# Kernel tuning notes

Measured on AMD Instinct MI355X. Metric: run time of the kernel, lower is better.

Reference implementation:

```python
import jax, jax.numpy as jnp
import numpy as np

EPS = 1e-5  # torch LayerNorm default

def _layernorm(x, g, b):
    mu = jnp.mean(x, axis=-1, keepdims=True)
    var = jnp.var(x, axis=-1, keepdims=True)
    return (x - mu) * jax.lax.rsqrt(var + EPS) * g + b

def _mlp(x, g, b, W1, b1, W2, b2):
    # pre-norm LayerNorm -> Linear -> SiLU -> Linear
    h = _layernorm(x, g, b)
    h = jax.nn.silu(h @ W1 + b1)
    return h @ W2 + b2

N, B, F, H = 500_000, 25_000, 128, 64

def setup_inputs() -> dict:
    key = jax.random.key(0)
    ks = jax.random.split(key, 16)
    s = 0.05
    return {
        "pos": jax.random.normal(ks[0], (N, 3), jnp.float32),
        "mass_center": jax.random.normal(ks[1], (B, 3), jnp.float32),
        "scaler": jax.random.normal(ks[2], (N, F), jnp.float32),
        "vector": jax.random.normal(ks[3], (N, 3, F), jnp.float32),
        "batch_index": jnp.sort(jax.random.randint(ks[4], (N,), 0, B)),
        # decoder_alpha params (pre-norm MLP F->H->1)
        "ln_a_g": jnp.ones((F,), jnp.float32),
        "ln_a_b": jnp.zeros((F,), jnp.float32),
        "Wa1": jax.random.normal(ks[5], (F, H), jnp.float32) * s,
        "ba1": jnp.zeros((H,), jnp.float32),
        "Wa2": jax.random.normal(ks[6], (H, 1), jnp.float32) * s,
        "ba2": jnp.zeros((1,), jnp.float32),
        # decoder_nu: gate MLP (pre-norm, F->H->1) + bias-free Linear(F,1)
        "ln_n_g": jnp.ones((F,), jnp.float32),
        "ln_n_b": jnp.zeros((F,), jnp.float32),
        "Wn1": jax.random.normal(ks[7], (F, H), jnp.float32) * s,
        "bn1": jnp.zeros((H,), jnp.float32),
        "Wn2": jax.random.normal(ks[8], (H, 1), jnp.float32) * s,
        "bn2": jnp.zeros((1,), jnp.float32),
        "Wnu": jax.random.normal(ks[9], (F, 1), jnp.float32) * s,
    }

def reference(pos, mass_center, scaler, vector, batch_index,
              ln_a_g, ln_a_b, Wa1, ba1, Wa2, ba2,
              ln_n_g, ln_n_b, Wn1, bn1, Wn2, bn2, Wnu):
    # gather per-node mass center and center positions: [N,3]
    mcv = pos - mass_center[batch_index]
    # Gate: mlp(scaler) [N,1] broadcast-multiplied with vector @ Wnu [N,3,1]
    s_gate = _mlp(scaler, ln_n_g, ln_n_b, Wn1, bn1, Wn2, bn2)       # [N,1]
    v_proj = jnp.einsum('ndf,fo->ndo', vector, Wnu)                  # [N,3,1]
    nu = (s_gate[:, None, :] * v_proj)[..., 0]                       # [N,3]
    # symmetric outer products: [N,3,3]
    outer = nu[:, :, None] * mcv[:, None, :] + mcv[:, :, None] * nu[:, None, :]
    alpha_s = _mlp(scaler, ln_a_g, ln_a_b, Wa1, ba1, Wa2, ba2)       # [N,1]
    alpha = alpha_s[:, :, None] * jnp.eye(3, dtype=alpha_s.dtype) + outer  # [N,3,3]
    # scatter-sum to molecule level, then trace/3
    mol = jax.ops.segment_sum(alpha, batch_index, num_segments=B)    # [B,3,3]
    out = jnp.einsum('bii->b', mol) / 3.0
    return out[:, None]                                              # [B,1]
```

## Files before the change

### kernel.cpp

```cpp
#include <hip/hip_runtime.h>

#define FD 128
#define HD 64
#define NC 128
#define RPB 64

typedef __attribute__((ext_vector_type(8))) short bf16x8;
typedef __attribute__((ext_vector_type(4))) float f32x4;

__device__ __forceinline__ unsigned bfr(float x) {
    unsigned u = __float_as_uint(x);
    return (u + 0x7fffu + ((u >> 16) & 1u)) >> 16;
}

__global__ void prep_kernel(
    const float* __restrict__ lnag, const float* __restrict__ lnab,
    const float* __restrict__ Wa1, const float* __restrict__ ba1, const float* __restrict__ Wa2,
    const float* __restrict__ lnng, const float* __restrict__ lnnb,
    const float* __restrict__ Wn1, const float* __restrict__ bn1, const float* __restrict__ Wn2,
    unsigned short* __restrict__ wq, float* __restrict__ c, float* __restrict__ w2)
{
    int n = threadIdx.x;
    const float* W  = (n < HD) ? Wa1 : Wn1;
    const float* g  = (n < HD) ? lnag : lnng;
    const float* bb = (n < HD) ? lnab : lnnb;
    const float* b1 = (n < HD) ? ba1 : bn1;
    const float* W2 = (n < HD) ? Wa2 : Wn2;
    int h = n & (HD - 1);
    float accb = b1[h];
    for (int f = 0; f < FD; ++f) {
        float w = W[f * HD + h];
        wq[n * FD + f] = (unsigned short)bfr(g[f] * w);
        accb += bb[f] * w;
    }
    c[n] = accb;
    w2[n] = W2[h];
}

__global__ __launch_bounds__(256) void fused_kernel(
    const float* __restrict__ scaler, const float* __restrict__ vec,
    const float* __restrict__ wnu, const float* __restrict__ pos,
    const float* __restrict__ mc, const int* __restrict__ bidx,
    const unsigned short* __restrict__ wq, const float* __restrict__ c,
    const float* __restrict__ w2, const float* __restrict__ ba2,
    const float* __restrict__ bn2, float* __restrict__ out, int n_nodes)
{
    __shared__ uint4 xs[RPB * 16];
    __shared__ float tl[RPB];

    int tid = threadIdx.x;
    int rowbase = blockIdx.x * RPB;
    int lane = tid & 63, w = tid >> 6;

    {
        int h = lane >> 5, j = lane & 31;
        float4 wn = reinterpret_cast<const float4*>(wnu)[j];
#pragma unroll
        for (int it = 0; it < 8; ++it) {
            int nl = w * 16 + it * 2 + h;
            int node = rowbase + nl;
            bool valid = node < n_nodes;
            int n = valid ? node : (n_nodes - 1);
            int b = bidx[n];
            float m0 = pos[n * 3 + 0] - mc[b * 3 + 0];
            float m1 = pos[n * 3 + 1] - mc[b * 3 + 1];
            float m2 = pos[n * 3 + 2] - mc[b * 3 + 2];
            const float4* vr = reinterpret_cast<const float4*>(vec + (size_t)n * 3 * FD);
            float4 v0 = vr[j], v1 = vr[32 + j], v2 = vr[64 + j];
            float acc = (v0.x * wn.x + v0.y * wn.y + v0.z * wn.z + v0.w * wn.w) * m0
                      + (v1.x * wn.x + v1.y * wn.y + v1.z * wn.z + v1.w * wn.w) * m1
                      + (v2.x * wn.x + v2.y * wn.y + v2.z * wn.z + v2.w * wn.w) * m2;
#pragma unroll
            for (int off = 16; off; off >>= 1) acc += __shfl_xor(acc, off);
            if (j == 0 && valid) tl[nl] = acc;
        }
    }

    {
        int r = tid >> 2, qd = tid & 3;
        int node = rowbase + r;
        int gn = node < n_nodes ? node : (n_nodes - 1);
        const float4* rp = reinterpret_cast<const float4*>(scaler + (size_t)gn * FD) + qd * 8;
        float4 v[8];
        float s = 0.f, s2 = 0.f;
#pragma unroll
        for (int i = 0; i < 8; ++i) {
            v[i] = rp[i];
            s  += v[i].x + v[i].y + v[i].z + v[i].w;
            s2 += v[i].x * v[i].x + v[i].y * v[i].y + v[i].z * v[i].z + v[i].w * v[i].w;
        }
        s  += __shfl_xor(s, 1);  s  += __shfl_xor(s, 2);
        s2 += __shfl_xor(s2, 1); s2 += __shfl_xor(s2, 2);
        float mu = s * (1.f / FD);
        float var = s2 * (1.f / FD) - mu * mu;
        float rstd = rsqrtf(var + 1e-5f);
#pragma unroll
        for (int jj = 0; jj < 4; ++jj) {
            float4 a = v[2 * jj], b = v[2 * jj + 1];
            uint4 pk;
            pk.x = bfr((a.x - mu) * rstd) | (bfr((a.y - mu) * rstd) << 16);
            pk.y = bfr((a.z - mu) * rstd) | (bfr((a.w - mu) * rstd) << 16);
            pk.z = bfr((b.x - mu) * rstd) | (bfr((b.y - mu) * rstd) << 16);
            pk.w = bfr((b.z - mu) * rstd) | (bfr((b.w - mu) * rstd) << 16);
            int slot = qd * 4 + jj;
            xs[r * 16 + (slot ^ (r & 15))] = pk;
        }
    }
    __syncthreads();

    int lrow = lane & 15, lgrp = lane >> 4;
    bf16x8 af[4];
#pragma unroll
    for (int ks = 0; ks < 4; ++ks) {
        int r = w * 16 + lrow;
        af[ks] = *reinterpret_cast<const bf16x8*>(&xs[r * 16 + ((ks * 4 + lgrp) ^ (r & 15))]);
    }
    float pa[4] = {0.f, 0.f, 0.f, 0.f}, pn[4] = {0.f, 0.f, 0.f, 0.f};
#pragma unroll
    for (int tile = 0; tile < 8; ++tile) {
        f32x4 acc = {0.f, 0.f, 0.f, 0.f};
        int n = tile * 16 + lrow;
        const bf16x8* brow = reinterpret_cast<const bf16x8*>(wq + n * FD);
#pragma unroll
        for (int ks = 0; ks < 4; ++ks) {
            bf16x8 bf = brow[ks * 4 + lgrp];
            acc = __builtin_amdgcn_mfma_f32_16x16x32_bf16(af[ks], bf, acc, 0, 0, 0);
        }
        int col = tile * 16 + lrow;
        float bias = c[col], w2v = w2[col];
#pragma unroll
        for (int r = 0; r < 4; ++r) {
            float h1 = acc[r] + bias;
            float y = h1 / (1.f + __expf(-h1));
            float cb = y * w2v;
            if (tile < 4) pa[r] += cb; else pn[r] += cb;
        }
    }
#pragma unroll
    for (int off = 1; off < 16; off <<= 1) {
#pragma unroll
        for (int r = 0; r < 4; ++r) {
            pa[r] += __shfl_xor(pa[r], off);
            pn[r] += __shfl_xor(pn[r], off);
        }
    }
    if (lrow == 0) {
        float b2a = ba2[0], b2n = bn2[0];
#pragma unroll
        for (int r = 0; r < 4; ++r) {
            int nl = w * 16 + lgrp * 4 + r;
            int node = rowbase + nl;
            if (node < n_nodes) {
                float val = (pa[r] + b2a) + (2.f / 3.f) * (pn[r] + b2n) * tl[nl];
                atomicAdd(out + bidx[node], val);
            }
        }
    }
}

extern "C" void kernel_launch(void* const* d_in, const int* in_sizes, int n_in,
                              void* d_out, int out_size, void* d_ws, size_t ws_size,
                              hipStream_t stream) {
    const float* pos    = (const float*)d_in[0];
    const float* mc     = (const float*)d_in[1];
    const float* scaler = (const float*)d_in[2];
    const float* vec    = (const float*)d_in[3];
    const int*   bidx   = (const int*)d_in[4];
    const float* lnag   = (const float*)d_in[5];
    const float* lnab   = (const float*)d_in[6];
    const float* Wa1    = (const float*)d_in[7];
    const float* ba1    = (const float*)d_in[8];
    const float* Wa2    = (const float*)d_in[9];
    const float* ba2    = (const float*)d_in[10];
    const float* lnng   = (const float*)d_in[11];
    const float* lnnb   = (const float*)d_in[12];
    const float* Wn1    = (const float*)d_in[13];
    const float* bn1    = (const float*)d_in[14];
    const float* Wn2    = (const float*)d_in[15];
    const float* bn2    = (const float*)d_in[16];
    const float* Wnu    = (const float*)d_in[17];

    int N = in_sizes[0] / 3;
    int B = in_sizes[1] / 3;

    unsigned short* wq = (unsigned short*)d_ws;
    float* c  = (float*)((char*)d_ws + NC * FD * 2);
    float* w2 = c + NC;

    hipMemsetAsync(d_out, 0, (size_t)B * sizeof(float), stream);

    hipLaunchKernelGGL(prep_kernel, dim3(1), dim3(NC), 0, stream,
                       lnag, lnab, Wa1, ba1, Wa2, lnng, lnnb, Wn1, bn1, Wn2, wq, c, w2);

    int blocks = (N + RPB - 1) / RPB;
    hipLaunchKernelGGL(fused_kernel, dim3(blocks), dim3(256), 0, stream,
                       scaler, vec, Wnu, pos, mc, bidx, wq, c, w2, ba2, bn2,
                       (float*)d_out, N);
}
```

Before: 277.6 us.

## Warp-specialize fused kernel into producer/consumer waves over persistent blocks

Turns the fused kernel into a persistent grid of 512 blocks with 512 threads each. Six producer waves stream the vector tensor and compute the per-node vector projection into a double-buffered shared slot. Two consumer waves do the LayerNorm, the MFMA MLP and the atomics, each handling 32 rows. The aim is to overlap the bandwidth-heavy vector reads with the scaler and MLP work and to cut per-block launch overhead. In exchange, only two waves now do all the scaler loads and MFMA work, occupancy drops to one block per CU, and every tile adds a block-wide barrier.

```diff
diff --git a/kernel.cpp b/kernel.cpp
--- a/kernel.cpp
+++ b/kernel.cpp
@@ -4,6 +4,8 @@
 #define HD 64
 #define NC 128
 #define RPB 64
+#define NPROD 6
+#define NBLK 512
 
 typedef __attribute__((ext_vector_type(8))) short bf16x8;
 typedef __attribute__((ext_vector_type(4))) float f32x4;
@@ -37,48 +39,43 @@
     w2[n] = W2[h];
 }
 
-__global__ __launch_bounds__(256) void fused_kernel(
-    const float* __restrict__ scaler, const float* __restrict__ vec,
-    const float* __restrict__ wnu, const float* __restrict__ pos,
-    const float* __restrict__ mc, const int* __restrict__ bidx,
-    const unsigned short* __restrict__ wq, const float* __restrict__ c,
-    const float* __restrict__ w2, const float* __restrict__ ba2,
-    const float* __restrict__ bn2, float* __restrict__ out, int n_nodes)
-{
-    __shared__ uint4 xs[RPB * 16];
-    __shared__ float tl[RPB];
-
-    int tid = threadIdx.x;
-    int rowbase = blockIdx.x * RPB;
-    int lane = tid & 63, w = tid >> 6;
-
-    {
-        int h = lane >> 5, j = lane & 31;
-        float4 wn = reinterpret_cast<const float4*>(wnu)[j];
-#pragma unroll
-        for (int it = 0; it < 8; ++it) {
-            int nl = w * 16 + it * 2 + h;
-            int node = rowbase + nl;
-            bool valid = node < n_nodes;
-            int n = valid ? node : (n_nodes - 1);
-            int b = bidx[n];
-            float m0 = pos[n * 3 + 0] - mc[b * 3 + 0];
-            float m1 = pos[n * 3 + 1] - mc[b * 3 + 1];
-            float m2 = pos[n * 3 + 2] - mc[b * 3 + 2];
-            const float4* vr = reinterpret_cast<const float4*>(vec + (size_t)n * 3 * FD);
-            float4 v0 = vr[j], v1 = vr[32 + j], v2 = vr[64 + j];
-            float acc = (v0.x * wn.x + v0.y * wn.y + v0.z * wn.z + v0.w * wn.w) * m0
-                      + (v1.x * wn.x + v1.y * wn.y + v1.z * wn.z + v1.w * wn.w) * m1
-                      + (v2.x * wn.x + v2.y * wn.y + v2.z * wn.z + v2.w * wn.w) * m2;
-#pragma unroll
-            for (int off = 16; off; off >>= 1) acc += __shfl_xor(acc, off);
-            if (j == 0 && valid) tl[nl] = acc;
-        }
-    }
-
-    {
-        int r = tid >> 2, qd = tid & 3;
-        int node = rowbase + r;
+__device__ __forceinline__ void produce_tile(
+    int tilebase, float* __restrict__ tslot,
+    const float* __restrict__ vec, const float4 wn,
+    const float* __restrict__ pos, const float* __restrict__ mc,
+    const int* __restrict__ bidx, int n_nodes, int hw, int j)
+{
+    for (int slot = hw; slot < RPB; slot += 2 * NPROD) {
+        int node = tilebase + slot;
+        bool valid = node < n_nodes;
+        int n = valid ? node : (n_nodes - 1);
+        const float4* vr = reinterpret_cast<const float4*>(vec + (size_t)n * 3 * FD);
+        float4 v0 = vr[j], v1 = vr[32 + j], v2 = vr[64 + j];
+        int b = bidx[n];
+        float m0 = pos[n * 3 + 0] - mc[b * 3 + 0];
+        float m1 = pos[n * 3 + 1] - mc[b * 3 + 1];
+        float m2 = pos[n * 3 + 2] - mc[b * 3 + 2];
+        float acc = (v0.x * wn.x + v0.y * wn.y + v0.z * wn.z + v0.w * wn.w) * m0
+                  + (v1.x * wn.x + v1.y * wn.y + v1.z * wn.z + v1.w * wn.w) * m1
+                  + (v2.x * wn.x + v2.y * wn.y + v2.z * wn.z + v2.w * wn.w) * m2;
+#pragma unroll
+        for (int off = 16; off; off >>= 1) acc += __shfl_xor(acc, off);
+        if (j == 0 && valid) tslot[slot] = acc;
+    }
+}
+
+__device__ __forceinline__ void consume_tile(
+    int tilebase, const float* __restrict__ tslot, uint4* __restrict__ xs,
+    const float* __restrict__ scaler, const unsigned short* __restrict__ wq,
+    const float* __restrict__ c, const float* __restrict__ w2,
+    float b2a, float b2n, const int* __restrict__ bidx,
+    float* __restrict__ out, int n_nodes, int cw, int lane)
+{
+    int r16 = lane >> 2, qd = lane & 3;
+#pragma unroll
+    for (int g = 0; g < 2; ++g) {
+        int row = cw * 32 + g * 16 + r16;
+        int node = tilebase + row;
         int gn = node < n_nodes ? node : (n_nodes - 1);
         const float4* rp = reinterpret_cast<const float4*>(scaler + (size_t)gn * FD) + qd * 8;
         float4 v[8];
@@ -103,57 +100,109 @@
             pk.z = bfr((b.x - mu) * rstd) | (bfr((b.y - mu) * rstd) << 16);
             pk.w = bfr((b.z - mu) * rstd) | (bfr((b.w - mu) * rstd) << 16);
             int slot = qd * 4 + jj;
-            xs[r * 16 + (slot ^ (r & 15))] = pk;
-        }
-    }
-    __syncthreads();
-
+            xs[row * 16 + (slot ^ (row & 15))] = pk;
+        }
+    }
     int lrow = lane & 15, lgrp = lane >> 4;
-    bf16x8 af[4];
+    bf16x8 af0[4], af1[4];
+    int r0 = cw * 32 + lrow, r1 = r0 + 16;
 #pragma unroll
     for (int ks = 0; ks < 4; ++ks) {
-        int r = w * 16 + lrow;
-        af[ks] = *reinterpret_cast<const bf16x8*>(&xs[r * 16 + ((ks * 4 + lgrp) ^ (r & 15))]);
-    }
-    float pa[4] = {0.f, 0.f, 0.f, 0.f}, pn[4] = {0.f, 0.f, 0.f, 0.f};
-#pragma unroll
-    for (int tile = 0; tile < 8; ++tile) {
-        f32x4 acc = {0.f, 0.f, 0.f, 0.f};
-        int n = tile * 16 + lrow;
+        af0[ks] = *reinterpret_cast<const bf16x8*>(&xs[r0 * 16 + ((ks * 4 + lgrp) ^ (r0 & 15))]);
+        af1[ks] = *reinterpret_cast<const bf16x8*>(&xs[r1 * 16 + ((ks * 4 + lgrp) ^ (r1 & 15))]);
+    }
+    float pa0[4] = {0,0,0,0}, pn0[4] = {0,0,0,0}, pa1[4] = {0,0,0,0}, pn1[4] = {0,0,0,0};
+#pragma unroll
+    for (int tc = 0; tc < 8; ++tc) {
+        f32x4 a0 = {0.f,0.f,0.f,0.f}, a1 = {0.f,0.f,0.f,0.f};
+        int n = tc * 16 + lrow;
         const bf16x8* brow = reinterpret_cast<const bf16x8*>(wq + n * FD);
 #pragma unroll
         for (int ks = 0; ks < 4; ++ks) {
             bf16x8 bf = brow[ks * 4 + lgrp];
-            acc = __builtin_amdgcn_mfma_f32_16x16x32_bf16(af[ks], bf, acc, 0, 0, 0);
-        }
-        int col = tile * 16 + lrow;
+            a0 = __builtin_amdgcn_mfma_f32_16x16x32_bf16(af0[ks], bf, a0, 0, 0, 0);
+            a1 = __builtin_amdgcn_mfma_f32_16x16x32_bf16(af1[ks], bf, a1, 0, 0, 0);
+        }
+        int col = tc * 16 + lrow;
         float bias = c[col], w2v = w2[col];
 #pragma unroll
         for (int r = 0; r < 4; ++r) {
-            float h1 = acc[r] + bias;
-            float y = h1 / (1.f + __expf(-h1));
-            float cb = y * w2v;
-            if (tile < 4) pa[r] += cb; else pn[r] += cb;
+            float h0 = a0[r] + bias, h1 = a1[r] + bias;
+            float y0 = h0 / (1.f + __expf(-h0));
+            float y1 = h1 / (1.f + __expf(-h1));
+            if (tc < 4) { pa0[r] += y0 * w2v; pa1[r] += y1 * w2v; }
+            else        { pn0[r] += y0 * w2v; pn1[r] += y1 * w2v; }
         }
     }
 #pragma unroll
     for (int off = 1; off < 16; off <<= 1) {
 #pragma unroll
         for (int r = 0; r < 4; ++r) {
-            pa[r] += __shfl_xor(pa[r], off);
-            pn[r] += __shfl_xor(pn[r], off);
+            pa0[r] += __shfl_xor(pa0[r], off);
+            pn0[r] += __shfl_xor(pn0[r], off);
+            pa1[r] += __shfl_xor(pa1[r], off);
+            pn1[r] += __shfl_xor(pn1[r], off);
         }
     }
     if (lrow == 0) {
-        float b2a = ba2[0], b2n = bn2[0];
 #pragma unroll
         for (int r = 0; r < 4; ++r) {
-            int nl = w * 16 + lgrp * 4 + r;
-            int node = rowbase + nl;
+            int row = cw * 32 + lgrp * 4 + r;
+            int node = tilebase + row;
             if (node < n_nodes) {
-                float val = (pa[r] + b2a) + (2.f / 3.f) * (pn[r] + b2n) * tl[nl];
+                float val = (pa0[r] + b2a) + (2.f / 3.f) * (pn0[r] + b2n) * tslot[row];
                 atomicAdd(out + bidx[node], val);
             }
+            int rowb = row + 16, nodeb = node + 16;
+            if (nodeb < n_nodes) {
+                float val = (pa1[r] + b2a) + (2.f / 3.f) * (pn1[r] + b2n) * tslot[rowb];
+                atomicAdd(out + bidx[nodeb], val);
+            }
+        }
+    }
+}
+
+__global__ __launch_bounds__(512, 1) void fused_kernel(
+    const float* __restrict__ scaler, const float* __restrict__ vec,
+    const float* __restrict__ wnu, const float* __restrict__ pos,
+    const float* __restrict__ mc, const int* __restrict__ bidx,
+    const unsigned short* __restrict__ wq, const float* __restrict__ c,
+    const float* __restrict__ w2, const float* __restrict__ ba2,
+    const float* __restrict__ bn2, float* __restrict__ out,
+    int n_nodes, int ntiles, int nblocks)
+{
+    __shared__ uint4 xs[RPB * 16];
+    __shared__ float tl[2][RPB];
+
+    int tid = threadIdx.x;
+    int lane = tid & 63;
+    int wid = tid >> 6;
+
+    int t0 = (int)(((long long)blockIdx.x * ntiles) / nblocks);
+    int t1 = (int)(((long long)(blockIdx.x + 1) * ntiles) / nblocks);
+    int m = t1 - t0;
+    if (m <= 0) return;
+
+    if (wid < NPROD) {
+        int hw = wid * 2 + (lane >> 5);
+        int j = lane & 31;
+        float4 wn = reinterpret_cast<const float4*>(wnu)[j];
+        produce_tile(t0 * RPB, tl[0], vec, wn, pos, mc, bidx, n_nodes, hw, j);
+        __syncthreads();
+        for (int k = 0; k < m; ++k) {
+            if (k + 1 < m)
+                produce_tile((t0 + k + 1) * RPB, tl[(k + 1) & 1], vec, wn, pos, mc, bidx,
+                             n_nodes, hw, j);
+            __syncthreads();
+        }
+    } else {
+        int cw = wid - NPROD;
+        float b2a = ba2[0], b2n = bn2[0];
+        __syncthreads();
+        for (int k = 0; k < m; ++k) {
+            consume_tile((t0 + k) * RPB, tl[k & 1], xs, scaler, wq, c, w2,
+                         b2a, b2n, bidx, out, n_nodes, cw, lane);
+            __syncthreads();
         }
     }
 }
@@ -192,8 +241,9 @@
     hipLaunchKernelGGL(prep_kernel, dim3(1), dim3(NC), 0, stream,
                        lnag, lnab, Wa1, ba1, Wa2, lnng, lnnb, Wn1, bn1, Wn2, wq, c, w2);
 
-    int blocks = (N + RPB - 1) / RPB;
-    hipLaunchKernelGGL(fused_kernel, dim3(blocks), dim3(256), 0, stream,
+    int ntiles = (N + RPB - 1) / RPB;
+    int nblocks = ntiles < NBLK ? ntiles : NBLK;
+    hipLaunchKernelGGL(fused_kernel, dim3(nblocks), dim3(512), 0, stream,
                        scaler, vec, Wnu, pos, mc, bidx, wq, c, w2, ba2, bn2,
-                       (float*)d_out, N);
-}
+                       (float*)d_out, N, ntiles, nblocks);
+}
```

Measured after the change: 381.8 us. 37.5% more time.
